# Kernel tuning notes

Measured on AMD Instinct MI355X. Metric: run time of the kernel, lower is better.

Reference implementation:

```python
import jax, jax.numpy as jnp
import numpy as np

B, S, D, H = 2, 2048, 1024, 16
DH = D // H
SCALE = DH ** -0.5


def setup_inputs() -> dict:
    key = jax.random.key(0)
    ks = jax.random.split(key, 12)
    std = D ** -0.5
    return {
        "Q": jax.random.normal(ks[0], (B, S, D), jnp.float32),
        "K": jax.random.normal(ks[1], (B, S, D), jnp.float32),
        "V": jax.random.normal(ks[2], (B, S, D), jnp.float32),
        "mask": jnp.ones((B, S), jnp.int32),
        "Wq": jax.random.normal(ks[3], (D, D), jnp.float32) * std,
        "bq": jnp.zeros((D,), jnp.float32),
        "Wk": jax.random.normal(ks[4], (D, D), jnp.float32) * std,
        "bk": jnp.zeros((D,), jnp.float32),
        "Wv": jax.random.normal(ks[5], (D, D), jnp.float32) * std,
        "bv": jnp.zeros((D,), jnp.float32),
        "Wo": jax.random.normal(ks[6], (D, D), jnp.float32) * std,
        "bo": jnp.zeros((D,), jnp.float32),
    }


def reference(Q, K, V, mask, Wq, bq, Wk, bk, Wv, bv, Wo, bo):
    b, s, d = Q.shape
    # QKV projections (nn.Linear: x @ W.T + b), split into heads -> [b,h,s,dh]
    q = (Q @ Wq.T + bq).reshape(b, s, H, DH).transpose(0, 2, 1, 3)
    k = (K @ Wk.T + bk).reshape(b, s, H, DH).transpose(0, 2, 1, 3)
    v = (V @ Wv.T + bv).reshape(b, s, H, DH).transpose(0, 2, 1, 3)
    # full O(S^2) score matrix, as in the original (non-flash)
    scores = jnp.einsum("bhqd,bhkd->bhqk", q, k) * SCALE
    # padding mask: [b,1,1,s]
    scores = jnp.where(mask[:, None, None, :] == 0, -jnp.inf, scores)
    # causal mask (causal=True)
    causal = jnp.arange(s)[:, None] >= jnp.arange(s)[None, :]
    scores = jnp.where(causal[None, None], scores, -jnp.inf)
    attn = jax.nn.softmax(scores, axis=-1)
    out = jnp.einsum("bhqk,bhkd->bhqd", attn, v)
    out = out.transpose(0, 2, 1, 3).reshape(b, s, d)
    return out @ Wo.T + bo  # dropout p=0 -> identity
```

## Files before the change

kernel.cpp:

```cpp
#include <hip/hip_runtime.h>
#include <hip/hip_bf16.h>
#include <math.h>

#define Bc  2
#define Sc  2048
#define Dc  1024
#define Hc  16
#define DHc 64
#define QSCALE 0.1803368801111244f

typedef __attribute__((ext_vector_type(8))) short short8;
typedef __attribute__((ext_vector_type(4))) float f32x4;

__device__ inline f32x4 mfma16(short8 a, short8 b, f32x4 c) {
    return __builtin_amdgcn_mfma_f32_16x16x32_bf16(a, b, c, 0, 0, 0);
}

typedef __attribute__((address_space(1))) const unsigned int g_u32;
typedef __attribute__((address_space(3))) unsigned int l_u32;
__device__ inline void gld16(const void* g, void* l) {
    __builtin_amdgcn_global_load_lds((g_u32*)g, (l_u32*)l, 16, 0, 0);
}

__device__ inline float fast_exp2(float x) { return __builtin_amdgcn_exp2f(x); }

__device__ inline short8 cvt8(float4 a, float4 b) {
    union { __hip_bfloat16 h[8]; short8 s; } u;
    u.h[0] = __float2bfloat16(a.x); u.h[1] = __float2bfloat16(a.y);
    u.h[2] = __float2bfloat16(a.z); u.h[3] = __float2bfloat16(a.w);
    u.h[4] = __float2bfloat16(b.x); u.h[5] = __float2bfloat16(b.y);
    u.h[6] = __float2bfloat16(b.z); u.h[7] = __float2bfloat16(b.w);
    return u.s;
}

__global__ __launch_bounds__(256) void castall_k(const float* __restrict__ W0, const float* __restrict__ W1,
                                                 const float* __restrict__ W2, const float* __restrict__ W3,
                                                 const float* __restrict__ I0, const float* __restrict__ I1,
                                                 const float* __restrict__ I2,
                                                 __hip_bfloat16* o0, __hip_bfloat16* o1,
                                                 __hip_bfloat16* o2, __hip_bfloat16* o3,
                                                 __hip_bfloat16* o4, __hip_bfloat16* o5,
                                                 __hip_bfloat16* o6)
{
    const int y = blockIdx.y;
    const float* s; __hip_bfloat16* d; size_t n;
    switch (y) {
        case 0: s = W0; d = o0; n = 1u << 20; break;
        case 1: s = W1; d = o1; n = 1u << 20; break;
        case 2: s = W2; d = o2; n = 1u << 20; break;
        case 3: s = W3; d = o3; n = 1u << 20; break;
        case 4: s = I0; d = o4; n = 1u << 22; break;
        case 5: s = I1; d = o5; n = 1u << 22; break;
        default: s = I2; d = o6; n = 1u << 22; break;
    }
    size_t idx = ((size_t)blockIdx.x * 256 + threadIdx.x) * 8;
    if (idx >= n) return;
    float4 a = *(const float4*)(s + idx);
    float4 b = *(const float4*)(s + idx + 4);
    *(short8*)(d + idx) = cvt8(a, b);
}

__global__ __launch_bounds__(256, 3) void qkv_k(const __hip_bfloat16* __restrict__ Qb,
                                                const __hip_bfloat16* __restrict__ Kb,
                                                const __hip_bfloat16* __restrict__ Vb,
                                                const __hip_bfloat16* __restrict__ Wqb,
                                                const __hip_bfloat16* __restrict__ Wkb,
                                                const __hip_bfloat16* __restrict__ Wvb,
                                                const float* __restrict__ bq, const float* __restrict__ bk,
                                                const float* __restrict__ bv,
                                                __hip_bfloat16* __restrict__ qo, __hip_bfloat16* __restrict__ ko,
                                                __hip_bfloat16* __restrict__ vto)
{
    __shared__ __align__(16) __hip_bfloat16 As[128 * 64];
    __shared__ __align__(16) __hip_bfloat16 Bs[128 * 64];
    const int p   = blockIdx.x >> 8;
    const int blk = blockIdx.x & 255;
    const int bm  = blk & 31, bn = blk >> 5;
    const __hip_bfloat16* A = p == 0 ? Qb : p == 1 ? Kb : Vb;
    const __hip_bfloat16* W = p == 0 ? Wqb : p == 1 ? Wkb : Wvb;
    const float* bias = p == 0 ? bq : p == 1 ? bk : bv;

    const int tid = threadIdx.x, wave = tid >> 6, lane = tid & 63;
    const int quad = lane >> 4, l15 = lane & 15;
    const int wm = wave >> 1, wn = wave & 1;
    const int sw = l15 & 7;

    f32x4 acc[4][4] = {};

#pragma unroll
    for (int i = 0; i < 4; ++i) {
        int c = wave * 64 + i * 256 + lane;
        int row = c >> 3, g = (c & 7) ^ (row & 7);
        gld16(A + (size_t)(bm * 128 + row) * 1024 + g * 8, (char*)As + (size_t)c * 16);
        gld16(W + (size_t)(bn * 128 + row) * 1024 + g * 8, (char*)Bs + (size_t)c * 16);
    }

    for (int kki = 0; kki < 16; ++kki) {
        __syncthreads();

        short8 af[4][2], bf2[4][2];
#pragma unroll
        for (int mi = 0; mi < 4; ++mi)
#pragma unroll
            for (int h = 0; h < 2; ++h)
                af[mi][h] = *(const short8*)((char*)As + (size_t)(wm * 64 + mi * 16 + l15) * 128 +
                                             ((((h << 2) + quad) ^ sw) << 4));
#pragma unroll
        for (int ni = 0; ni < 4; ++ni)
#pragma unroll
            for (int h = 0; h < 2; ++h)
                bf2[ni][h] = *(const short8*)((char*)Bs + (size_t)(wn * 64 + ni * 16 + l15) * 128 +
                                              ((((h << 2) + quad) ^ sw) << 4));

        __syncthreads();

        if (kki < 15) {
            const int kk2 = (kki + 1) * 64;
#pragma unroll
            for (int i = 0; i < 4; ++i) {
                int c = wave * 64 + i * 256 + lane;
                int row = c >> 3, g = (c & 7) ^ (row & 7);
                gld16(A + (size_t)(bm * 128 + row) * 1024 + kk2 + g * 8, (char*)As + (size_t)c * 16);
                gld16(W + (size_t)(bn * 128 + row) * 1024 + kk2 + g * 8, (char*)Bs + (size_t)c * 16);
            }
        }

#pragma unroll
        for (int mi = 0; mi < 4; ++mi)
#pragma unroll
            for (int ni = 0; ni < 4; ++ni) {
                acc[mi][ni] = mfma16(af[mi][0], bf2[ni][0], acc[mi][ni]);
                acc[mi][ni] = mfma16(af[mi][1], bf2[ni][1], acc[mi][ni]);
            }
    }

    float bvv[4];
#pragma unroll
    for (int ni = 0; ni < 4; ++ni) bvv[ni] = bias[bn * 128 + wn * 64 + ni * 16 + l15];
#pragma unroll
    for (int mi = 0; mi < 4; ++mi) {
#pragma unroll
        for (int r = 0; r < 4; ++r) {
            int m = bm * 128 + wm * 64 + mi * 16 + quad * 4 + r;
            int b_ = m >> 11, s_ = m & 2047;
#pragma unroll
            for (int ni = 0; ni < 4; ++ni) {
                int n = bn * 128 + wn * 64 + ni * 16 + l15;
                int h_ = n >> 6, d_ = n & 63;
                float val = acc[mi][ni][r] + bvv[ni];
                if (p == 0) val *= QSCALE;
                __hip_bfloat16 hv = __float2bfloat16(val);
                if (p < 2) {
                    __hip_bfloat16* dst = (p == 0 ? qo : ko);
                    dst[((size_t)(b_ * Hc + h_) * Sc + s_) * DHc + d_] = hv;
                } else {
                    int loc = s_ & 63;
                    int sp = (s_ & ~63) | ((loc & 15) << 2) | (loc >> 4);
                    vto[((size_t)(b_ * Hc + h_) * DHc + d_) * Sc + sp] = hv;
                }
            }
        }
    }
}

__global__ __launch_bounds__(256, 3) void attn_k(const __hip_bfloat16* __restrict__ qb,
                                                 const __hip_bfloat16* __restrict__ kb,
                                                 const __hip_bfloat16* __restrict__ vtb,
                                                 const int* __restrict__ mask,
                                                 __hip_bfloat16* __restrict__ obE,
                                                 __hip_bfloat16* __restrict__ obO,
                                                 float* __restrict__ lsE,
                                                 float* __restrict__ lsO)
{
    __shared__ __align__(16) __hip_bfloat16 Klds[2][64 * 64];
    __shared__ __align__(16) __hip_bfloat16 Vlds[2][64 * 64];
    __shared__ __align__(16) __hip_bfloat16 Plds[4][32 * 72];

    const int bh = blockIdx.x & 31;
    const int kp = (blockIdx.x >> 5) & 1;
    const int qt = 15 - (blockIdx.x >> 6);
    const int b  = bh >> 4;
    const int tid = threadIdx.x, wave = tid >> 6, lane = tid & 63;
    const int quad = lane >> 4, l15 = lane & 15;
    const int sw = l15 & 7;
    const int r0 = qt * 128 + wave * 32;

    const __hip_bfloat16* qh  = qb  + (size_t)bh * Sc * DHc;
    const __hip_bfloat16* kh  = kb  + (size_t)bh * Sc * DHc;
    const __hip_bfloat16* vth = vtb + (size_t)bh * DHc * Sc;
    __hip_bfloat16* obP = kp ? obO : obE;
    float*           lsP = kp ? lsO : lsE;

    short8 qf[2][2];
#pragma unroll
    for (int rc = 0; rc < 2; ++rc)
#pragma unroll
        for (int h = 0; h < 2; ++h)
            qf[rc][h] = *(const short8*)(qh + (size_t)(r0 + rc * 16 + l15) * DHc + h * 32 + quad * 8);

    f32x4 O[2][4] = {};
    float lsum[2][4] = {};

    {
        const int kv = kp * 64;
#pragma unroll
        for (int i = 0; i < 2; ++i) {
            int c = i * 256 + wave * 64 + lane;
            int row = c >> 3, g = (c & 7) ^ (row & 7);
            gld16(kh + (size_t)(kv + row) * DHc + g * 8, (char*)&Klds[0][0] + (size_t)c * 16);
            gld16(vth + (size_t)row * Sc + kv + g * 8, (char*)&Vlds[0][0] + (size_t)c * 16);
        }
    }

    for (int j = 0; j <= qt; ++j) {
        __syncthreads();
        if (j < qt) {
            const int kv1 = (kp + 2 * (j + 1)) * 64, nb = (j + 1) & 1;
#pragma unroll
            for (int i = 0; i < 2; ++i) {
                int c = i * 256 + wave * 64 + lane;
                int row = c >> 3, g = (c & 7) ^ (row & 7);
                gld16(kh + (size_t)(kv1 + row) * DHc + g * 8, (char*)&Klds[nb][0] + (size_t)c * 16);
                gld16(vth + (size_t)row * Sc + kv1 + g * 8, (char*)&Vlds[nb][0] + (size_t)c * 16);
            }
        }
        const int kv0 = (kp + 2 * j) * 64, buf = j & 1;
        if (kv0 >= r0 + 32) continue;

        f32x4 sc[2][4] = {};
#pragma unroll
        for (int h = 0; h < 2; ++h)
#pragma unroll
            for (int nc = 0; nc < 4; ++nc) {
                short8 kf = *(const short8*)((char*)&Klds[buf][0] +
                            (size_t)(nc * 16 + l15) * 128 + ((((h << 2) + quad) ^ sw) << 4));
                sc[0][nc] = mfma16(qf[0][h], kf, sc[0][nc]);
                sc[1][nc] = mfma16(qf[1][h], kf, sc[1][nc]);
            }

        float mb[4];
#pragma unroll
        for (int nc = 0; nc < 4; ++nc)
            mb[nc] = mask[b * Sc + kv0 + nc * 16 + l15] ? 0.f : -__builtin_inff();

        if (kv0 + 64 > r0) {
#pragma unroll
            for (int rc = 0; rc < 2; ++rc)
#pragma unroll
                for (int r = 0; r < 4; ++r) {
                    const int q_idx = r0 + rc * 16 + quad * 4 + r;
                    float pv[4], ps = 0.f;
#pragma unroll
                    for (int nc = 0; nc < 4; ++nc) {
                        int key = kv0 + nc * 16 + l15;
                        float s = sc[rc][nc][r] + mb[nc];
                        s = (key <= q_idx) ? s : -__builtin_inff();
                        pv[nc] = fast_exp2(fminf(s, 43.f));
                        ps += pv[nc];
                    }
                    lsum[rc][r] += ps;
                    union { __hip_bfloat16 h[4]; unsigned long long u; } pp;
#pragma unroll
                    for (int nc = 0; nc < 4; ++nc) pp.h[nc] = __float2bfloat16(pv[nc]);
                    *(unsigned long long*)((char*)&Plds[wave][0] +
                        (size_t)(rc * 16 + quad * 4 + r) * 144 + l15 * 8) = pp.u;
                }
        } else {
#pragma unroll
            for (int rc = 0; rc < 2; ++rc)
#pragma unroll
                for (int r = 0; r < 4; ++r) {
                    float pv[4], ps = 0.f;
#pragma unroll
                    for (int nc = 0; nc < 4; ++nc) {
                        float s = sc[rc][nc][r] + mb[nc];
                        pv[nc] = fast_exp2(fminf(s, 43.f));
                        ps += pv[nc];
                    }
                    lsum[rc][r] += ps;
                    union { __hip_bfloat16 h[4]; unsigned long long u; } pp;
#pragma unroll
                    for (int nc = 0; nc < 4; ++nc) pp.h[nc] = __float2bfloat16(pv[nc]);
                    *(unsigned long long*)((char*)&Plds[wave][0] +
                        (size_t)(rc * 16 + quad * 4 + r) * 144 + l15 * 8) = pp.u;
                }
        }

#pragma unroll
        for (int h = 0; h < 2; ++h) {
            short8 pf0 = *(const short8*)((char*)&Plds[wave][0] + (size_t)l15 * 144 + h * 64 + quad * 16);
            short8 pf1 = *(const short8*)((char*)&Plds[wave][0] + (size_t)(16 + l15) * 144 + h * 64 + quad * 16);
#pragma unroll
            for (int nc = 0; nc < 4; ++nc) {
                short8 vf = *(const short8*)((char*)&Vlds[buf][0] +
                            (size_t)(nc * 16 + l15) * 128 + ((((h << 2) + quad) ^ sw) << 4));
                O[0][nc] = mfma16(pf0, vf, O[0][nc]);
                O[1][nc] = mfma16(pf1, vf, O[1][nc]);
            }
        }
    }

#pragma unroll
    for (int rc = 0; rc < 2; ++rc)
#pragma unroll
        for (int r = 0; r < 4; ++r) {
            float l = lsum[rc][r];
#pragma unroll
            for (int off = 1; off < 16; off <<= 1) l += __shfl_xor(l, off);
            const int q_idx = r0 + rc * 16 + quad * 4 + r;
            if (l15 == 0) lsP[(size_t)bh * Sc + q_idx] = l;
#pragma unroll
            for (int nc = 0; nc < 4; ++nc)
                obP[((size_t)bh * Sc + q_idx) * DHc + nc * 16 + l15] =
                    __float2bfloat16(O[rc][nc][r]);
        }
}

__global__ __launch_bounds__(256) void combine_k(const __hip_bfloat16* __restrict__ Oe,
                                                 const __hip_bfloat16* __restrict__ Oo,
                                                 const float* __restrict__ le,
                                                 const float* __restrict__ lo,
                                                 __hip_bfloat16* __restrict__ out)
{
    size_t t = (size_t)blockIdx.x * 256 + threadIdx.x;
    size_t row = t >> 3;
    float inv = 1.f / (le[row] + lo[row]);
    union { short8 s; __hip_bfloat16 h[8]; } ua, ub, uo;
    ua.s = *(const short8*)(Oe + t * 8);
    ub.s = *(const short8*)(Oo + t * 8);
#pragma unroll
    for (int i = 0; i < 8; ++i)
        uo.h[i] = __float2bfloat16((__bfloat162float(ua.h[i]) + __bfloat162float(ub.h[i])) * inv);
    *(short8*)(out + t * 8) = uo.s;
}

__global__ __launch_bounds__(256, 4) void out_k(const __hip_bfloat16* __restrict__ Ab,
                                                const __hip_bfloat16* __restrict__ Wb,
                                                const float* __restrict__ bias,
                                                float* __restrict__ outp)
{
    __shared__ __align__(16) __hip_bfloat16 As[128 * 64];
    __shared__ __align__(16) __hip_bfloat16 Bs[64 * 64];
    const int bm = blockIdx.x & 31, bn = blockIdx.x >> 5;
    const int tid = threadIdx.x, wave = tid >> 6, lane = tid & 63;
    const int quad = lane >> 4, l15 = lane & 15;
    const int wm = wave >> 1, wn = wave & 1;
    const int sw = l15 & 7;

    f32x4 acc[4][2] = {};

#pragma unroll
    for (int i = 0; i < 4; ++i) {
        int c = wave * 64 + i * 256 + lane;
        int row = c >> 3, g = (c & 7) ^ (row & 7);
        int m = bm * 128 + row, b_ = m >> 11, s_ = m & 2047;
        gld16(Ab + (((size_t)(b_ * Hc) * Sc + s_) * DHc + g * 8), (char*)As + (size_t)c * 16);
    }
#pragma unroll
    for (int i = 0; i < 2; ++i) {
        int c = wave * 64 + i * 256 + lane;
        int row = c >> 3, g = (c & 7) ^ (row & 7);
        gld16(Wb + (size_t)(bn * 64 + row) * 1024 + g * 8, (char*)Bs + (size_t)c * 16);
    }

    for (int kki = 0; kki < 16; ++kki) {
        __syncthreads();

        short8 af[4][2], bf2[2][2];
#pragma unroll
        for (int mi = 0; mi < 4; ++mi)
#pragma unroll
            for (int h = 0; h < 2; ++h)
                af[mi][h] = *(const short8*)((char*)As + (size_t)(wm * 64 + mi * 16 + l15) * 128 +
                                             ((((h << 2) + quad) ^ sw) << 4));
#pragma unroll
        for (int ni = 0; ni < 2; ++ni)
#pragma unroll
            for (int h = 0; h < 2; ++h)
                bf2[ni][h] = *(const short8*)((char*)Bs + (size_t)(wn * 32 + ni * 16 + l15) * 128 +
                                              ((((h << 2) + quad) ^ sw) << 4));

        __syncthreads();

        if (kki < 15) {
            const int h2 = kki + 1, kk2 = h2 * 64;
#pragma unroll
            for (int i = 0; i < 4; ++i) {
                int c = wave * 64 + i * 256 + lane;
                int row = c >> 3, g = (c & 7) ^ (row & 7);
                int m = bm * 128 + row, b_ = m >> 11, s_ = m & 2047;
                gld16(Ab + (((size_t)(b_ * Hc + h2) * Sc + s_) * DHc + g * 8), (char*)As + (size_t)c * 16);
            }
#pragma unroll
            for (int i = 0; i < 2; ++i) {
                int c = wave * 64 + i * 256 + lane;
                int row = c >> 3, g = (c & 7) ^ (row & 7);
                gld16(Wb + (size_t)(bn * 64 + row) * 1024 + kk2 + g * 8, (char*)Bs + (size_t)c * 16);
            }
        }

#pragma unroll
        for (int mi = 0; mi < 4; ++mi)
#pragma unroll
            for (int ni = 0; ni < 2; ++ni) {
                acc[mi][ni] = mfma16(af[mi][0], bf2[ni][0], acc[mi][ni]);
                acc[mi][ni] = mfma16(af[mi][1], bf2[ni][1], acc[mi][ni]);
            }
    }

    float bvv[2];
#pragma unroll
    for (int ni = 0; ni < 2; ++ni) bvv[ni] = bias[bn * 64 + wn * 32 + ni * 16 + l15];
#pragma unroll
    for (int mi = 0; mi < 4; ++mi)
#pragma unroll
        for (int r = 0; r < 4; ++r) {
            int m = bm * 128 + wm * 64 + mi * 16 + quad * 4 + r;
#pragma unroll
            for (int ni = 0; ni < 2; ++ni) {
                int n = bn * 64 + wn * 32 + ni * 16 + l15;
                outp[(size_t)m * 1024 + n] = acc[mi][ni][r] + bvv[ni];
            }
        }
}

extern "C" void kernel_launch(void* const* d_in, const int* in_sizes, int n_in,
                              void* d_out, int out_size, void* d_ws, size_t ws_size,
                              hipStream_t stream) {
    const float* Q   = (const float*)d_in[0];
    const float* K   = (const float*)d_in[1];
    const float* V   = (const float*)d_in[2];
    const int*  mask = (const int*)d_in[3];
    const float* Wq  = (const float*)d_in[4];
    const float* bq  = (const float*)d_in[5];
    const float* Wk  = (const float*)d_in[6];
    const float* bk  = (const float*)d_in[7];
    const float* Wv  = (const float*)d_in[8];
    const float* bv  = (const float*)d_in[9];
    const float* Wo  = (const float*)d_in[10];
    const float* bo  = (const float*)d_in[11];

    char* ws = (char*)d_ws;
    __hip_bfloat16* wqb = (__hip_bfloat16*)(ws);
    __hip_bfloat16* wkb = (__hip_bfloat16*)(ws + (2u << 20));
    __hip_bfloat16* wvb = (__hip_bfloat16*)(ws + (4u << 20));
    __hip_bfloat16* wob = (__hip_bfloat16*)(ws + (6u << 20));
    __hip_bfloat16* qbuf  = (__hip_bfloat16*)(ws + (8u << 20));
    __hip_bfloat16* kbuf  = (__hip_bfloat16*)(ws + (16u << 20));
    __hip_bfloat16* vtbuf = (__hip_bfloat16*)(ws + (24u << 20));
    __hip_bfloat16* Qbf   = (__hip_bfloat16*)(ws + (32u << 20));
    __hip_bfloat16* Kbf   = (__hip_bfloat16*)(ws + (40u << 20));
    __hip_bfloat16* Vbf   = (__hip_bfloat16*)(ws + (48u << 20));
    __hip_bfloat16* Oe    = Qbf;
    __hip_bfloat16* Oo    = Kbf;
    float* lsE = (float*)(ws + (48u << 20));
    float* lsO = (float*)(ws + (48u << 20) + (256u << 10));

    castall_k<<<dim3(2048, 7), 256, 0, stream>>>(Wq, Wk, Wv, Wo, Q, K, V,
                                                 wqb, wkb, wvb, wob, Qbf, Kbf, Vbf);
    qkv_k<<<768, 256, 0, stream>>>(Qbf, Kbf, Vbf, wqb, wkb, wvb, bq, bk, bv, qbuf, kbuf, vtbuf);
    attn_k<<<1024, 256, 0, stream>>>(qbuf, kbuf, vtbuf, mask, Oe, Oo, lsE, lsO);
    combine_k<<<2048, 256, 0, stream>>>(Oe, Oo, lsE, lsO, qbuf);
    out_k<<<512, 256, 0, stream>>>(qbuf, wob, bo, (float*)d_out);
}
```

Before: 209.0 us.

## Fuse fp32-to-bf16 activation cast into QKV projection GEMM loads

The QKV GEMM now reads fp32 Q/K/V directly, converts to bf16 in registers and writes swizzled tiles to LDS, with the next tile's loads issued before the MFMAs and the stores after them. The separate cast kernel now handles only the four weight matrices. This removes a full write and re-read of 24M bf16 activation elements. In exchange, A-tile loads go through registers instead of async global-to-LDS loads, which raises register pressure and reads each activation element from fp32 global memory 8 times, once per N-block.

```diff
diff --git a/kernel.cpp b/kernel.cpp
--- a/kernel.cpp
+++ b/kernel.cpp
@@ -33,36 +33,22 @@
     return u.s;
 }
 
-__global__ __launch_bounds__(256) void castall_k(const float* __restrict__ W0, const float* __restrict__ W1,
-                                                 const float* __restrict__ W2, const float* __restrict__ W3,
-                                                 const float* __restrict__ I0, const float* __restrict__ I1,
-                                                 const float* __restrict__ I2,
-                                                 __hip_bfloat16* o0, __hip_bfloat16* o1,
-                                                 __hip_bfloat16* o2, __hip_bfloat16* o3,
-                                                 __hip_bfloat16* o4, __hip_bfloat16* o5,
-                                                 __hip_bfloat16* o6)
+__global__ __launch_bounds__(256) void castw_k(const float* __restrict__ W0, const float* __restrict__ W1,
+                                               const float* __restrict__ W2, const float* __restrict__ W3,
+                                               __hip_bfloat16* o0, __hip_bfloat16* o1,
+                                               __hip_bfloat16* o2, __hip_bfloat16* o3)
 {
-    const int y = blockIdx.y;
-    const float* s; __hip_bfloat16* d; size_t n;
-    switch (y) {
-        case 0: s = W0; d = o0; n = 1u << 20; break;
-        case 1: s = W1; d = o1; n = 1u << 20; break;
-        case 2: s = W2; d = o2; n = 1u << 20; break;
-        case 3: s = W3; d = o3; n = 1u << 20; break;
-        case 4: s = I0; d = o4; n = 1u << 22; break;
-        case 5: s = I1; d = o5; n = 1u << 22; break;
-        default: s = I2; d = o6; n = 1u << 22; break;
-    }
+    const float* s = blockIdx.y == 0 ? W0 : blockIdx.y == 1 ? W1 : blockIdx.y == 2 ? W2 : W3;
+    __hip_bfloat16* d = blockIdx.y == 0 ? o0 : blockIdx.y == 1 ? o1 : blockIdx.y == 2 ? o2 : o3;
     size_t idx = ((size_t)blockIdx.x * 256 + threadIdx.x) * 8;
-    if (idx >= n) return;
     float4 a = *(const float4*)(s + idx);
     float4 b = *(const float4*)(s + idx + 4);
     *(short8*)(d + idx) = cvt8(a, b);
 }
 
-__global__ __launch_bounds__(256, 3) void qkv_k(const __hip_bfloat16* __restrict__ Qb,
-                                                const __hip_bfloat16* __restrict__ Kb,
-                                                const __hip_bfloat16* __restrict__ Vb,
+__global__ __launch_bounds__(256, 3) void qkv_k(const float* __restrict__ Qf,
+                                                const float* __restrict__ Kf,
+                                                const float* __restrict__ Vf,
                                                 const __hip_bfloat16* __restrict__ Wqb,
                                                 const __hip_bfloat16* __restrict__ Wkb,
                                                 const __hip_bfloat16* __restrict__ Wvb,
@@ -76,7 +62,7 @@
     const int p   = blockIdx.x >> 8;
     const int blk = blockIdx.x & 255;
     const int bm  = blk & 31, bn = blk >> 5;
-    const __hip_bfloat16* A = p == 0 ? Qb : p == 1 ? Kb : Vb;
+    const float* A = p == 0 ? Qf : p == 1 ? Kf : Vf;
     const __hip_bfloat16* W = p == 0 ? Wqb : p == 1 ? Wkb : Wvb;
     const float* bias = p == 0 ? bq : p == 1 ? bk : bv;
 
@@ -85,14 +71,29 @@
     const int wm = wave >> 1, wn = wave & 1;
     const int sw = l15 & 7;
 
+    int arow[4], acc_[4];
+    const float* asrc[4];
+#pragma unroll
+    for (int i = 0; i < 4; ++i) {
+        int c = tid + i * 256;
+        arow[i] = c >> 3; acc_[i] = c & 7;
+        int g = acc_[i] ^ (arow[i] & 7);
+        asrc[i] = A + (size_t)(bm * 128 + arow[i]) * 1024 + g * 8;
+    }
+
     f32x4 acc[4][4] = {};
 
 #pragma unroll
     for (int i = 0; i < 4; ++i) {
         int c = wave * 64 + i * 256 + lane;
         int row = c >> 3, g = (c & 7) ^ (row & 7);
-        gld16(A + (size_t)(bm * 128 + row) * 1024 + g * 8, (char*)As + (size_t)c * 16);
         gld16(W + (size_t)(bn * 128 + row) * 1024 + g * 8, (char*)Bs + (size_t)c * 16);
+    }
+#pragma unroll
+    for (int i = 0; i < 4; ++i) {
+        float4 v0 = *(const float4*)(asrc[i]);
+        float4 v1 = *(const float4*)(asrc[i] + 4);
+        *(short8*)((char*)As + (size_t)arow[i] * 128 + acc_[i] * 16) = cvt8(v0, v1);
     }
 
     for (int kki = 0; kki < 16; ++kki) {
@@ -114,14 +115,19 @@
 
         __syncthreads();
 
+        float4 va[4][2];
         if (kki < 15) {
             const int kk2 = (kki + 1) * 64;
 #pragma unroll
             for (int i = 0; i < 4; ++i) {
                 int c = wave * 64 + i * 256 + lane;
                 int row = c >> 3, g = (c & 7) ^ (row & 7);
-                gld16(A + (size_t)(bm * 128 + row) * 1024 + kk2 + g * 8, (char*)As + (size_t)c * 16);
                 gld16(W + (size_t)(bn * 128 + row) * 1024 + kk2 + g * 8, (char*)Bs + (size_t)c * 16);
+            }
+#pragma unroll
+            for (int i = 0; i < 4; ++i) {
+                va[i][0] = *(const float4*)(asrc[i] + kk2);
+                va[i][1] = *(const float4*)(asrc[i] + kk2 + 4);
             }
         }
 
@@ -132,6 +138,12 @@
                 acc[mi][ni] = mfma16(af[mi][0], bf2[ni][0], acc[mi][ni]);
                 acc[mi][ni] = mfma16(af[mi][1], bf2[ni][1], acc[mi][ni]);
             }
+
+        if (kki < 15) {
+#pragma unroll
+            for (int i = 0; i < 4; ++i)
+                *(short8*)((char*)As + (size_t)arow[i] * 128 + acc_[i] * 16) = cvt8(va[i][0], va[i][1]);
+        }
     }
 
     float bvv[4];
@@ -448,17 +460,13 @@
     __hip_bfloat16* qbuf  = (__hip_bfloat16*)(ws + (8u << 20));
     __hip_bfloat16* kbuf  = (__hip_bfloat16*)(ws + (16u << 20));
     __hip_bfloat16* vtbuf = (__hip_bfloat16*)(ws + (24u << 20));
-    __hip_bfloat16* Qbf   = (__hip_bfloat16*)(ws + (32u << 20));
-    __hip_bfloat16* Kbf   = (__hip_bfloat16*)(ws + (40u << 20));
-    __hip_bfloat16* Vbf   = (__hip_bfloat16*)(ws + (48u << 20));
-    __hip_bfloat16* Oe    = Qbf;
-    __hip_bfloat16* Oo    = Kbf;
+    __hip_bfloat16* Oe    = (__hip_bfloat16*)(ws + (32u << 20));
+    __hip_bfloat16* Oo    = (__hip_bfloat16*)(ws + (40u << 20));
     float* lsE = (float*)(ws + (48u << 20));
     float* lsO = (float*)(ws + (48u << 20) + (256u << 10));
 
-    castall_k<<<dim3(2048, 7), 256, 0, stream>>>(Wq, Wk, Wv, Wo, Q, K, V,
-                                                 wqb, wkb, wvb, wob, Qbf, Kbf, Vbf);
-    qkv_k<<<768, 256, 0, stream>>>(Qbf, Kbf, Vbf, wqb, wkb, wvb, bq, bk, bv, qbuf, kbuf, vtbuf);
+    castw_k<<<dim3(512, 4), 256, 0, stream>>>(Wq, Wk, Wv, Wo, wqb, wkb, wvb, wob);
+    qkv_k<<<768, 256, 0, stream>>>(Q, K, V, wqb, wkb, wvb, bq, bk, bv, qbuf, kbuf, vtbuf);
     attn_k<<<1024, 256, 0, stream>>>(qbuf, kbuf, vtbuf, mask, Oe, Oo, lsE, lsO);
     combine_k<<<2048, 256, 0, stream>>>(Oe, Oo, lsE, lsO, qbuf);
     out_k<<<512, 256, 0, stream>>>(qbuf, wob, bo, (float*)d_out);
```

Result: slower. 226.5 us (+8.4%).

## Fuse split-KV combine into attention kernel via atomic last-block reduction

Applied to the files above, without the earlier changes.

The separate combine kernel is removed. The two key-parity partial results are now merged inside the attention kernel. Each block publishes its partial O and row sums, bumps a per-tile atomic counter and, if it arrives second, reads the sibling's partial to write the normalized output directly. This removes one kernel launch and a full pass over both partial buffers, at the cost of counter zeroing in the cast kernel, threadfences and an extra dependent global read in the finishing block.

```diff
diff --git a/kernel.cpp b/kernel.cpp
--- a/kernel.cpp
+++ b/kernel.cpp
@@ -40,9 +40,13 @@
                                                  __hip_bfloat16* o0, __hip_bfloat16* o1,
                                                  __hip_bfloat16* o2, __hip_bfloat16* o3,
                                                  __hip_bfloat16* o4, __hip_bfloat16* o5,
-                                                 __hip_bfloat16* o6)
+                                                 __hip_bfloat16* o6,
+                                                 int* __restrict__ cnt)
 {
     const int y = blockIdx.y;
+    if (y == 0 && blockIdx.x == 0) {
+        if (threadIdx.x < 256) { cnt[threadIdx.x] = 0; cnt[threadIdx.x + 256] = 0; }
+    }
     const float* s; __hip_bfloat16* d; size_t n;
     switch (y) {
         case 0: s = W0; d = o0; n = 1u << 20; break;
@@ -170,15 +174,19 @@
                                                  __hip_bfloat16* __restrict__ obE,
                                                  __hip_bfloat16* __restrict__ obO,
                                                  float* __restrict__ lsE,
-                                                 float* __restrict__ lsO)
+                                                 float* __restrict__ lsO,
+                                                 int* __restrict__ cnt,
+                                                 __hip_bfloat16* __restrict__ ofinal)
 {
     __shared__ __align__(16) __hip_bfloat16 Klds[2][64 * 64];
     __shared__ __align__(16) __hip_bfloat16 Vlds[2][64 * 64];
     __shared__ __align__(16) __hip_bfloat16 Plds[4][32 * 72];
+    __shared__ int last;
 
     const int bh = blockIdx.x & 31;
     const int kp = (blockIdx.x >> 5) & 1;
     const int qt = 15 - (blockIdx.x >> 6);
+    const int pid = (blockIdx.x >> 6) * 32 + bh;
     const int b  = bh >> 4;
     const int tid = threadIdx.x, wave = tid >> 6, lane = tid & 63;
     const int quad = lane >> 4, l15 = lane & 15;
@@ -212,9 +220,10 @@
         }
     }
 
-    for (int j = 0; j <= qt; ++j) {
+    const int nkt = qt + 1;
+    for (int j = 0; j < nkt; ++j) {
         __syncthreads();
-        if (j < qt) {
+        if (j + 1 < nkt) {
             const int kv1 = (kp + 2 * (j + 1)) * 64, nb = (j + 1) & 1;
 #pragma unroll
             for (int i = 0; i < 2; ++i) {
@@ -300,6 +309,7 @@
         }
     }
 
+    float lred[2][4];
 #pragma unroll
     for (int rc = 0; rc < 2; ++rc)
 #pragma unroll
@@ -307,31 +317,46 @@
             float l = lsum[rc][r];
 #pragma unroll
             for (int off = 1; off < 16; off <<= 1) l += __shfl_xor(l, off);
+            lred[rc][r] = l;
+        }
+
+#pragma unroll
+    for (int rc = 0; rc < 2; ++rc)
+#pragma unroll
+        for (int r = 0; r < 4; ++r) {
             const int q_idx = r0 + rc * 16 + quad * 4 + r;
-            if (l15 == 0) lsP[(size_t)bh * Sc + q_idx] = l;
+            if (l15 == 0) lsP[(size_t)bh * Sc + q_idx] = lred[rc][r];
 #pragma unroll
             for (int nc = 0; nc < 4; ++nc)
                 obP[((size_t)bh * Sc + q_idx) * DHc + nc * 16 + l15] =
                     __float2bfloat16(O[rc][nc][r]);
         }
-}
-
-__global__ __launch_bounds__(256) void combine_k(const __hip_bfloat16* __restrict__ Oe,
-                                                 const __hip_bfloat16* __restrict__ Oo,
-                                                 const float* __restrict__ le,
-                                                 const float* __restrict__ lo,
-                                                 __hip_bfloat16* __restrict__ out)
-{
-    size_t t = (size_t)blockIdx.x * 256 + threadIdx.x;
-    size_t row = t >> 3;
-    float inv = 1.f / (le[row] + lo[row]);
-    union { short8 s; __hip_bfloat16 h[8]; } ua, ub, uo;
-    ua.s = *(const short8*)(Oe + t * 8);
-    ub.s = *(const short8*)(Oo + t * 8);
-#pragma unroll
-    for (int i = 0; i < 8; ++i)
-        uo.h[i] = __float2bfloat16((__bfloat162float(ua.h[i]) + __bfloat162float(ub.h[i])) * inv);
-    *(short8*)(out + t * 8) = uo.s;
+
+    __threadfence();
+    __syncthreads();
+    if (tid == 0) last = atomicAdd(&cnt[pid], 1);
+    __syncthreads();
+
+    if (last == 1) {
+        __threadfence();
+        const __hip_bfloat16* obQ = kp ? obE : obO;
+        const float*          lsQ = kp ? lsE : lsO;
+#pragma unroll
+        for (int rc = 0; rc < 2; ++rc)
+#pragma unroll
+            for (int r = 0; r < 4; ++r) {
+                const int q_idx = r0 + rc * 16 + quad * 4 + r;
+                const float lo = lsQ[(size_t)bh * Sc + q_idx];
+                const float inv = 1.f / (lred[rc][r] + lo);
+#pragma unroll
+                for (int nc = 0; nc < 4; ++nc) {
+                    float v = O[rc][nc][r] +
+                        __bfloat162float(obQ[((size_t)bh * Sc + q_idx) * DHc + nc * 16 + l15]);
+                    ofinal[((size_t)bh * Sc + q_idx) * DHc + nc * 16 + l15] =
+                        __float2bfloat16(v * inv);
+                }
+            }
+    }
 }
 
 __global__ __launch_bounds__(256, 4) void out_k(const __hip_bfloat16* __restrict__ Ab,
@@ -451,15 +476,13 @@
     __hip_bfloat16* Qbf   = (__hip_bfloat16*)(ws + (32u << 20));
     __hip_bfloat16* Kbf   = (__hip_bfloat16*)(ws + (40u << 20));
     __hip_bfloat16* Vbf   = (__hip_bfloat16*)(ws + (48u << 20));
-    __hip_bfloat16* Oe    = Qbf;
-    __hip_bfloat16* Oo    = Kbf;
-    float* lsE = (float*)(ws + (48u << 20));
-    float* lsO = (float*)(ws + (48u << 20) + (256u << 10));
+    float* lsE = (float*)(ws + (56u << 20));
+    float* lsO = (float*)(ws + (56u << 20) + (256u << 10));
+    int*   cnt = (int*)(ws + (56u << 20) + (512u << 10));
 
     castall_k<<<dim3(2048, 7), 256, 0, stream>>>(Wq, Wk, Wv, Wo, Q, K, V,
-                                                 wqb, wkb, wvb, wob, Qbf, Kbf, Vbf);
+                                                 wqb, wkb, wvb, wob, Qbf, Kbf, Vbf, cnt);
     qkv_k<<<768, 256, 0, stream>>>(Qbf, Kbf, Vbf, wqb, wkb, wvb, bq, bk, bv, qbuf, kbuf, vtbuf);
-    attn_k<<<1024, 256, 0, stream>>>(qbuf, kbuf, vtbuf, mask, Oe, Oo, lsE, lsO);
-    combine_k<<<2048, 256, 0, stream>>>(Oe, Oo, lsE, lsO, qbuf);
+    attn_k<<<1024, 256, 0, stream>>>(qbuf, kbuf, vtbuf, mask, Qbf, Kbf, lsE, lsO, cnt, qbuf);
     out_k<<<512, 256, 0, stream>>>(qbuf, wob, bo, (float*)d_out);
 }
```

After: 414.6 us. 98.4% more time.

## Enlarge attention query tile to 256 rows with per-16-row causal skipping

Applied to the files above, without the earlier changes.

Each attention block now covers 256 query rows, with 64 per wave, instead of 128, and the grid is halved. Every K/V tile loaded into LDS is therefore reused across twice as many query rows, which cuts global and LDS load traffic per unit of work. The inner loop is restructured to process one 16-row chunk at a time, skip chunks that lie fully above the causal diagonal, and use a smaller P buffer. The cost is more accumulator registers per thread, which may reduce occupancy under the 3-block launch bound, and fewer blocks with a larger causal imbalance between them.

```diff
diff --git a/kernel.cpp b/kernel.cpp
--- a/kernel.cpp
+++ b/kernel.cpp
@@ -174,16 +174,16 @@
 {
     __shared__ __align__(16) __hip_bfloat16 Klds[2][64 * 64];
     __shared__ __align__(16) __hip_bfloat16 Vlds[2][64 * 64];
-    __shared__ __align__(16) __hip_bfloat16 Plds[4][32 * 72];
+    __shared__ __align__(16) __hip_bfloat16 Plds[4][16 * 72];
 
     const int bh = blockIdx.x & 31;
     const int kp = (blockIdx.x >> 5) & 1;
-    const int qt = 15 - (blockIdx.x >> 6);
+    const int qs = 7 - (blockIdx.x >> 6);
     const int b  = bh >> 4;
     const int tid = threadIdx.x, wave = tid >> 6, lane = tid & 63;
     const int quad = lane >> 4, l15 = lane & 15;
     const int sw = l15 & 7;
-    const int r0 = qt * 128 + wave * 32;
+    const int r0 = qs * 256 + wave * 64;
 
     const __hip_bfloat16* qh  = qb  + (size_t)bh * Sc * DHc;
     const __hip_bfloat16* kh  = kb  + (size_t)bh * Sc * DHc;
@@ -191,15 +191,17 @@
     __hip_bfloat16* obP = kp ? obO : obE;
     float*           lsP = kp ? lsO : lsE;
 
-    short8 qf[2][2];
-#pragma unroll
-    for (int rc = 0; rc < 2; ++rc)
+    short8 qf[4][2];
+#pragma unroll
+    for (int rc = 0; rc < 4; ++rc)
 #pragma unroll
         for (int h = 0; h < 2; ++h)
             qf[rc][h] = *(const short8*)(qh + (size_t)(r0 + rc * 16 + l15) * DHc + h * 32 + quad * 8);
 
-    f32x4 O[2][4] = {};
-    float lsum[2][4] = {};
+    f32x4 O[4][4] = {};
+    float lsum[4][4] = {};
+
+    const int nkt = 2 * qs + 2;
 
     {
         const int kv = kp * 64;
@@ -212,9 +214,9 @@
         }
     }
 
-    for (int j = 0; j <= qt; ++j) {
+    for (int j = 0; j < nkt; ++j) {
         __syncthreads();
-        if (j < qt) {
+        if (j + 1 < nkt) {
             const int kv1 = (kp + 2 * (j + 1)) * 64, nb = (j + 1) & 1;
 #pragma unroll
             for (int i = 0; i < 2; ++i) {
@@ -225,35 +227,37 @@
             }
         }
         const int kv0 = (kp + 2 * j) * 64, buf = j & 1;
-        if (kv0 >= r0 + 32) continue;
-
-        f32x4 sc[2][4] = {};
-#pragma unroll
-        for (int h = 0; h < 2; ++h)
-#pragma unroll
-            for (int nc = 0; nc < 4; ++nc) {
-                short8 kf = *(const short8*)((char*)&Klds[buf][0] +
-                            (size_t)(nc * 16 + l15) * 128 + ((((h << 2) + quad) ^ sw) << 4));
-                sc[0][nc] = mfma16(qf[0][h], kf, sc[0][nc]);
-                sc[1][nc] = mfma16(qf[1][h], kf, sc[1][nc]);
-            }
+        if (kv0 >= r0 + 64) continue;
 
         float mb[4];
 #pragma unroll
         for (int nc = 0; nc < 4; ++nc)
             mb[nc] = mask[b * Sc + kv0 + nc * 16 + l15] ? 0.f : -__builtin_inff();
 
-        if (kv0 + 64 > r0) {
-#pragma unroll
-            for (int rc = 0; rc < 2; ++rc)
+#pragma unroll
+        for (int rc = 0; rc < 4; ++rc) {
+            const int rrc = r0 + rc * 16;
+            if (kv0 >= rrc + 16) continue;
+
+            f32x4 sc[4] = {};
+#pragma unroll
+            for (int h = 0; h < 2; ++h)
+#pragma unroll
+                for (int nc = 0; nc < 4; ++nc) {
+                    short8 kf = *(const short8*)((char*)&Klds[buf][0] +
+                                (size_t)(nc * 16 + l15) * 128 + ((((h << 2) + quad) ^ sw) << 4));
+                    sc[nc] = mfma16(qf[rc][h], kf, sc[nc]);
+                }
+
+            if (kv0 + 64 > rrc) {
 #pragma unroll
                 for (int r = 0; r < 4; ++r) {
-                    const int q_idx = r0 + rc * 16 + quad * 4 + r;
+                    const int q_idx = rrc + quad * 4 + r;
                     float pv[4], ps = 0.f;
 #pragma unroll
                     for (int nc = 0; nc < 4; ++nc) {
                         int key = kv0 + nc * 16 + l15;
-                        float s = sc[rc][nc][r] + mb[nc];
+                        float s = sc[nc][r] + mb[nc];
                         s = (key <= q_idx) ? s : -__builtin_inff();
                         pv[nc] = fast_exp2(fminf(s, 43.f));
                         ps += pv[nc];
@@ -263,17 +267,15 @@
 #pragma unroll
                     for (int nc = 0; nc < 4; ++nc) pp.h[nc] = __float2bfloat16(pv[nc]);
                     *(unsigned long long*)((char*)&Plds[wave][0] +
-                        (size_t)(rc * 16 + quad * 4 + r) * 144 + l15 * 8) = pp.u;
+                        (size_t)(quad * 4 + r) * 144 + l15 * 8) = pp.u;
                 }
-        } else {
-#pragma unroll
-            for (int rc = 0; rc < 2; ++rc)
+            } else {
 #pragma unroll
                 for (int r = 0; r < 4; ++r) {
                     float pv[4], ps = 0.f;
 #pragma unroll
                     for (int nc = 0; nc < 4; ++nc) {
-                        float s = sc[rc][nc][r] + mb[nc];
+                        float s = sc[nc][r] + mb[nc];
                         pv[nc] = fast_exp2(fminf(s, 43.f));
                         ps += pv[nc];
                     }
@@ -282,26 +284,25 @@
 #pragma unroll
                     for (int nc = 0; nc < 4; ++nc) pp.h[nc] = __float2bfloat16(pv[nc]);
                     *(unsigned long long*)((char*)&Plds[wave][0] +
-                        (size_t)(rc * 16 + quad * 4 + r) * 144 + l15 * 8) = pp.u;
+                        (size_t)(quad * 4 + r) * 144 + l15 * 8) = pp.u;
                 }
-        }
-
-#pragma unroll
-        for (int h = 0; h < 2; ++h) {
-            short8 pf0 = *(const short8*)((char*)&Plds[wave][0] + (size_t)l15 * 144 + h * 64 + quad * 16);
-            short8 pf1 = *(const short8*)((char*)&Plds[wave][0] + (size_t)(16 + l15) * 144 + h * 64 + quad * 16);
-#pragma unroll
-            for (int nc = 0; nc < 4; ++nc) {
-                short8 vf = *(const short8*)((char*)&Vlds[buf][0] +
-                            (size_t)(nc * 16 + l15) * 128 + ((((h << 2) + quad) ^ sw) << 4));
-                O[0][nc] = mfma16(pf0, vf, O[0][nc]);
-                O[1][nc] = mfma16(pf1, vf, O[1][nc]);
-            }
-        }
-    }
-
-#pragma unroll
-    for (int rc = 0; rc < 2; ++rc)
+            }
+
+#pragma unroll
+            for (int h = 0; h < 2; ++h) {
+                short8 pf = *(const short8*)((char*)&Plds[wave][0] + (size_t)l15 * 144 + h * 64 + quad * 16);
+#pragma unroll
+                for (int nc = 0; nc < 4; ++nc) {
+                    short8 vf = *(const short8*)((char*)&Vlds[buf][0] +
+                                (size_t)(nc * 16 + l15) * 128 + ((((h << 2) + quad) ^ sw) << 4));
+                    O[rc][nc] = mfma16(pf, vf, O[rc][nc]);
+                }
+            }
+        }
+    }
+
+#pragma unroll
+    for (int rc = 0; rc < 4; ++rc)
 #pragma unroll
         for (int r = 0; r < 4; ++r) {
             float l = lsum[rc][r];
@@ -459,7 +460,7 @@
     castall_k<<<dim3(2048, 7), 256, 0, stream>>>(Wq, Wk, Wv, Wo, Q, K, V,
                                                  wqb, wkb, wvb, wob, Qbf, Kbf, Vbf);
     qkv_k<<<768, 256, 0, stream>>>(Qbf, Kbf, Vbf, wqb, wkb, wvb, bq, bk, bv, qbuf, kbuf, vtbuf);
-    attn_k<<<1024, 256, 0, stream>>>(qbuf, kbuf, vtbuf, mask, Oe, Oo, lsE, lsO);
+    attn_k<<<512, 256, 0, stream>>>(qbuf, kbuf, vtbuf, mask, Oe, Oo, lsE, lsO);
     combine_k<<<2048, 256, 0, stream>>>(Oe, Oo, lsE, lsO, qbuf);
     out_k<<<512, 256, 0, stream>>>(qbuf, wob, bo, (float*)d_out);
 }
```

Result: slower. 240.7 us (+15.2%).
